# Kernel optimization log

Hardware: AMD Instinct MI355X
Metric: run time of the kernel (lower is better)

## Reference

```python
import jax, jax.numpy as jnp
import numpy as np

ALPHA = 0.2          # LeakyReLU slope
NEG_BIG = -9e15      # mask value from the torch code
LN_EPS = 1e-5        # torch LayerNorm default eps
GAT_SCALE = 1.0


def _layer_norm(x, g, b):
    mu = x.mean(-1, keepdims=True)
    var = ((x - mu) ** 2).mean(-1, keepdims=True)
    return (x - mu) * jax.lax.rsqrt(var + LN_EPS) * g + b


def _gat_layer(h, adj, W, a, concat):
    # h: [B,N,Fin], adj: [N,N] weighted, W: [Fin,Fout], a: [2*Fout,1]
    Wh = jnp.einsum('bnf,fo->bno', h, W)                 # [B,N,Fout]
    Fo = W.shape[1]
    a_i, a_j = a[:Fo, 0], a[Fo:, 0]
    # e[b,i,j] = leakyrelu(Wh[b,i].a_i + Wh[b,j].a_j)  (== cat([Wh_i,Wh_j]) @ a)
    e = jax.nn.leaky_relu(
        (Wh @ a_i)[:, :, None] + (Wh @ a_j)[:, None, :], ALPHA)  # [B,N,N]
    att = jnp.where(adj[None, :, :] > 0, e, NEG_BIG)
    att = jax.nn.softmax(att, axis=2)
    att = att * adj[None, :, :]
    att = att / (att.sum(axis=2, keepdims=True) + 1e-8)
    h_prime = jnp.einsum('bij,bjo->bio', att, Wh)        # [B,N,Fout]
    return jax.nn.elu(h_prime) if concat else h_prime


def setup_inputs() -> dict:
    B, N, H, ID = 1024, 128, 64, 8
    GIN = 1 + ID  # node_feat_dim = 0
    key = jax.random.key(0)
    ks = jax.random.split(key, 20)
    # sparse weighted adjacency with self-loops
    w = jax.random.uniform(ks[0], (N, N))
    m = (jax.random.uniform(ks[1], (N, N)) < 0.3).astype(jnp.float32)
    adj = w * m + jnp.eye(N, dtype=jnp.float32)
    sc = lambda k, s: jax.random.normal(k, s, jnp.float32) * 0.1
    return {
        'c_values': jax.random.normal(ks[2], (B, N), jnp.float32),
        'adj': adj,
        'agent_emb': sc(ks[3], (N, ID)),
        'W1': sc(ks[4], (GIN, H)), 'a1': sc(ks[5], (2 * H, 1)),
        'W2': sc(ks[6], (H, H)),   'a2': sc(ks[7], (2 * H, 1)),
        'ln1_g': jnp.ones((H,)), 'ln1_b': jnp.zeros((H,)),
        'ln2_g': jnp.ones((H,)), 'ln2_b': jnp.zeros((H,)),
        'head_gat_w': sc(ks[8], (H, 1)), 'head_gat_b': jnp.zeros((1,)),
        'mlp1_w': sc(ks[9], (N, H)),  'mlp1_b': jnp.zeros((H,)),
        'mlp2_w': sc(ks[10], (H, H)), 'mlp2_b': jnp.zeros((H,)),
        'head_mlp_w': sc(ks[11], (H, 1)), 'head_mlp_b': jnp.zeros((1,)),
        'gate1_w': sc(ks[12], (N, H)), 'gate1_b': jnp.zeros((H,)),
        'gate2_w': sc(ks[13], (H, 1)), 'gate2_b': jnp.full((1,), -5.0),
    }


def reference(c_values, adj, agent_emb, W1, a1, W2, a2,
              ln1_g, ln1_b, ln2_g, ln2_b, head_gat_w, head_gat_b,
              mlp1_w, mlp1_b, mlp2_w, mlp2_b, head_mlp_w, head_mlp_b,
              gate1_w, gate1_b, gate2_w, gate2_b):
    B, N = c_values.shape
    # node features: [c_value, agent_id_embedding]
    id_feat = jnp.broadcast_to(agent_emb[None], (B, N, agent_emb.shape[1]))
    x_g = jnp.concatenate([c_values[..., None], id_feat], axis=-1)  # [B,N,9]
    h1 = _gat_layer(x_g, adj, W1, a1, concat=True)
    h1 = _layer_norm(h1, ln1_g, ln1_b)
    h2 = _gat_layer(h1, adj, W2, a2, concat=False)
    h = jax.nn.relu(h2 + h1)
    h = _layer_norm(h, ln2_g, ln2_b)
    q_gat = h.mean(axis=1) @ head_gat_w + head_gat_b                # [B,1]
    x_m = jax.nn.relu(c_values @ mlp1_w + mlp1_b)
    x_m = jax.nn.relu(x_m @ mlp2_w + mlp2_b)
    q_mlp = x_m @ head_mlp_w + head_mlp_b                           # [B,1]
    gate = jax.nn.sigmoid(
        jax.nn.relu(c_values @ gate1_w + gate1_b) @ gate2_w + gate2_b)
    return q_mlp + gate * GAT_SCALE * q_gat
```

## Files before the change

### kernel.cpp

```cpp
#include <hip/hip_runtime.h>

typedef unsigned short u16;
typedef unsigned int u32;
typedef short v8s __attribute__((ext_vector_type(8)));
typedef float v4f __attribute__((ext_vector_type(4)));

__device__ __forceinline__ float bflo(u32 d){union{u32 i;float f;}u;u.i=d<<16;return u.f;}
__device__ __forceinline__ float bfhi(u32 d){union{u32 i;float f;}u;u.i=d&0xffff0000u;return u.f;}
__device__ __forceinline__ u16 f2bfr(float f){union{float f;u32 i;}u;u.f=f;return (u16)((u.i+0x8000u)>>16);}
__device__ __forceinline__ u32 pk2bf(float a,float b){
    union{float f;u32 i;}ua,ub; ua.f=a; ub.f=b;
    return ((ua.i+0x8000u)>>16)|((ub.i+0x8000u)&0xffff0000u);
}
__device__ __forceinline__ v8s pack8(const float* w){
    union { uint4 u; v8s v; } c;
    c.u.x = pk2bf(w[0],w[1]); c.u.y = pk2bf(w[2],w[3]);
    c.u.z = pk2bf(w[4],w[5]); c.u.w = pk2bf(w[6],w[7]);
    return c.v;
}

__device__ __forceinline__ void flash_att(
    int wv, int l15, int q4,
    const float* __restrict__ ADJ,
    const float* __restrict__ sEi, const float* __restrict__ sEj,
    const u16* __restrict__ sWhT,
    v4f acc[2][4], float invD[2])
{
    const int r0 = 16*wv + l15, r1 = r0 + 64;
    const float ei0 = sEi[r0], ei1 = sEi[r1];
    float D0 = 0.f, D1 = 0.f;
    #pragma unroll
    for (int s = 0; s < 2; ++s)
        #pragma unroll
        for (int ct = 0; ct < 4; ++ct) acc[s][ct] = (v4f){0.f,0.f,0.f,0.f};

    for (int ks = 0; ks < 4; ++ks) {
        const int ko = ks*32 + q4*8;
        float ej[8];
        *(float4*)(ej)     = *(const float4*)(sEj + ko);
        *(float4*)(ej + 4) = *(const float4*)(sEj + ko + 4);
        float4 a00 = *(const float4*)(ADJ + r0*128 + ko);
        float4 a01 = *(const float4*)(ADJ + r0*128 + ko + 4);
        float4 a10 = *(const float4*)(ADJ + r1*128 + ko);
        float4 a11 = *(const float4*)(ADJ + r1*128 + ko + 4);
        float av0[8] = {a00.x,a00.y,a00.z,a00.w,a01.x,a01.y,a01.z,a01.w};
        float av1[8] = {a10.x,a10.y,a10.z,a10.w,a11.x,a11.y,a11.z,a11.w};
        float w0[8], w1[8];
        #pragma unroll
        for (int k = 0; k < 8; ++k) {
            float e0 = ei0 + ej[k]; e0 = fmaxf(e0, 0.2f*e0);
            float e1 = ei1 + ej[k]; e1 = fmaxf(e1, 0.2f*e1);
            float x0 = __expf(e0) * av0[k];
            float x1 = __expf(e1) * av1[k];
            w0[k] = x0; w1[k] = x1; D0 += x0; D1 += x1;
        }
        v8s A0 = pack8(w0), A1 = pack8(w1);
        #pragma unroll
        for (int ct = 0; ct < 4; ++ct) {
            v8s B = *(const v8s*)(sWhT + (16*ct + l15)*136 + ko);
            acc[0][ct] = __builtin_amdgcn_mfma_f32_16x16x32_bf16(A0, B, acc[0][ct], 0,0,0);
            acc[1][ct] = __builtin_amdgcn_mfma_f32_16x16x32_bf16(A1, B, acc[1][ct], 0,0,0);
        }
    }
    D0 += __shfl_xor(D0, 16); D0 += __shfl_xor(D0, 32);
    D1 += __shfl_xor(D1, 16); D1 += __shfl_xor(D1, 32);
    invD[0] = 1.f / D0; invD[1] = 1.f / D1;
}

__global__ __launch_bounds__(256, 4) void graphmixer_kernel(
    const float* __restrict__ C,
    const float* __restrict__ ADJ,
    const float* __restrict__ EMB,
    const float* __restrict__ W1,
    const float* __restrict__ A1,
    const float* __restrict__ W2,
    const float* __restrict__ A2,
    const float* __restrict__ LN1G, const float* __restrict__ LN1B,
    const float* __restrict__ LN2G, const float* __restrict__ LN2B,
    const float* __restrict__ HGW,  const float* __restrict__ HGB,
    const float* __restrict__ MLP1W, const float* __restrict__ MLP1B,
    const float* __restrict__ MLP2W, const float* __restrict__ MLP2B,
    const float* __restrict__ HMW,  const float* __restrict__ HMB,
    const float* __restrict__ G1W,  const float* __restrict__ G1B,
    const float* __restrict__ G2W,  const float* __restrict__ G2B,
    float* __restrict__ OUT)
{
    const int b = blockIdx.x, t = threadIdx.x;
    const int lane = t & 63, wv = t >> 6;
    const int l15 = lane & 15, q4 = lane >> 4;

    __shared__ __align__(16) unsigned char smem[39072];
    u16*   sWhT = (u16*)(smem);
    u16*   sH1  = (u16*)(smem + 17408);
    float* sEi  = (float*)(smem + 35840);
    float* sEj  = (float*)(smem + 36352);
    float* colp = (float*)(smem + 36864);
    float* sScr = (float*)(smem + 37888);
    float* v2i  = (float*)(smem + 38432);
    float* v2j  = (float*)(smem + 38688);
    float* v1i  = (float*)(smem + 38944);
    float* v1j  = (float*)(smem + 39008);
    float* sEmb = (float*)(smem + 17408);
    float* sC   = (float*)(smem + 21504);

    const float* Cb = C + b*128;

    if (wv == 0) {
        #pragma unroll
        for (int q = 0; q < 4; ++q)
            ((float4*)sEmb)[lane + 64*q] = ((const float4*)EMB)[lane + 64*q];
        if (lane < 32) ((float4*)sC)[lane] = ((const float4*)Cb)[lane];
        if (lane >= 32 && lane < 41) {
            int f = lane - 32; float a = 0.f;
            for (int q = 0; q < 16; ++q) {
                float4 w = *(const float4*)(W1 + f*64 + q*4);
                float4 x = *(const float4*)(A1 + q*4);
                a += w.x*x.x + w.y*x.y + w.z*x.z + w.w*x.w;
            }
            v1i[f] = a;
        } else if (lane >= 48 && lane < 57) {
            int f = lane - 48; float a = 0.f;
            for (int q = 0; q < 16; ++q) {
                float4 w = *(const float4*)(W1 + f*64 + q*4);
                float4 x = *(const float4*)(A1 + 64 + q*4);
                a += w.x*x.x + w.y*x.y + w.z*x.z + w.w*x.w;
            }
            v1j[f] = a;
        }
    } else if (wv == 3) {
        float ai = 0.f, aj = 0.f;
        for (int q = 0; q < 16; ++q) {
            float4 w  = *(const float4*)(W2 + lane*64 + q*4);
            float4 xi = *(const float4*)(A2 + q*4);
            float4 xj = *(const float4*)(A2 + 64 + q*4);
            ai += w.x*xi.x + w.y*xi.y + w.z*xi.z + w.w*xi.w;
            aj += w.x*xj.x + w.y*xj.y + w.z*xj.z + w.w*xj.w;
        }
        v2i[lane] = ai; v2j[lane] = aj;
    } else if (wv == 1) {
        float a = 0.f;
        for (int k = 0; k < 128; k += 4) {
            float4 c4 = *(const float4*)(Cb + k);
            a += c4.x*MLP1W[k*64+lane] + c4.y*MLP1W[(k+1)*64+lane]
               + c4.z*MLP1W[(k+2)*64+lane] + c4.w*MLP1W[(k+3)*64+lane];
        }
        sScr[lane] = fmaxf(a + MLP1B[lane], 0.f);
        float a2 = 0.f;
        for (int k = 0; k < 64; ++k) a2 += sScr[k] * MLP2W[k*64 + lane];
        float x2 = fmaxf(a2 + MLP2B[lane], 0.f);
        float p1 = x2 * HMW[lane];
        #pragma unroll
        for (int off = 32; off >= 1; off >>= 1) p1 += __shfl_down(p1, off);
        if (lane == 0) sScr[128] = p1 + HMB[0];
    } else {
        float a = 0.f;
        for (int k = 0; k < 128; k += 4) {
            float4 c4 = *(const float4*)(Cb + k);
            a += c4.x*G1W[k*64+lane] + c4.y*G1W[(k+1)*64+lane]
               + c4.z*G1W[(k+2)*64+lane] + c4.w*G1W[(k+3)*64+lane];
        }
        sScr[64 + lane] = fmaxf(a + G1B[lane], 0.f);
        float p2 = sScr[64 + lane] * G2W[lane];
        #pragma unroll
        for (int off = 32; off >= 1; off >>= 1) p2 += __shfl_down(p2, off);
        if (lane == 0) sScr[129] = 1.f / (1.f + __expf(-(p2 + G2B[0])));
    }
    __syncthreads();

    {
        const int o = lane, cc = wv;
        float w1f[9];
        #pragma unroll
        for (int f = 0; f < 9; ++f) w1f[f] = W1[f*64 + o];
        float whv[32];
        for (int i = 0; i < 32; ++i) {
            const int ig = cc*32 + i;
            float a = sC[ig] * w1f[0];
            float4 e0 = *(const float4*)(sEmb + ig*8);
            float4 e1 = *(const float4*)(sEmb + ig*8 + 4);
            a += e0.x*w1f[1] + e0.y*w1f[2] + e0.z*w1f[3] + e0.w*w1f[4];
            a += e1.x*w1f[5] + e1.y*w1f[6] + e1.z*w1f[7] + e1.w*w1f[8];
            whv[i] = a;
        }
        u32 p[16];
        #pragma unroll
        for (int q = 0; q < 16; ++q) p[q] = pk2bf(whv[2*q], whv[2*q+1]);
        uint4* dst = (uint4*)(sWhT + o*136 + cc*32);
        dst[0] = ((uint4*)p)[0]; dst[1] = ((uint4*)p)[1];
        dst[2] = ((uint4*)p)[2]; dst[3] = ((uint4*)p)[3];
    }
    if (t < 128) {
        float c = sC[t];
        float4 e0 = *(const float4*)(sEmb + t*8);
        float4 e1 = *(const float4*)(sEmb + t*8 + 4);
        float ei = c*v1i[0] + e0.x*v1i[1]+e0.y*v1i[2]+e0.z*v1i[3]+e0.w*v1i[4]
                            + e1.x*v1i[5]+e1.y*v1i[6]+e1.z*v1i[7]+e1.w*v1i[8];
        float ej = c*v1j[0] + e0.x*v1j[1]+e0.y*v1j[2]+e0.z*v1j[3]+e0.w*v1j[4]
                            + e1.x*v1j[5]+e1.y*v1j[6]+e1.z*v1j[7]+e1.w*v1j[8];
        sEi[t] = ei; sEj[t] = ej;
    }
    __syncthreads();

    {
        v4f acc[2][4]; float invD[2];
        flash_att(wv, l15, q4, ADJ, sEi, sEj, sWhT, acc, invD);

        float g4[4], b4[4];
        #pragma unroll
        for (int ct = 0; ct < 4; ++ct) { g4[ct] = LN1G[16*ct + l15]; b4[ct] = LN1B[16*ct + l15]; }
        #pragma unroll
        for (int s = 0; s < 2; ++s) {
            const int rbase = 16*(wv + 4*s) + 4*q4;
            #pragma unroll
            for (int reg = 0; reg < 4; ++reg) {
                const int row = rbase + reg;
                const float rd = __shfl(invD[s], 4*q4 + reg);
                float x[4], s1 = 0.f, s2 = 0.f;
                #pragma unroll
                for (int ct = 0; ct < 4; ++ct) {
                    float v = acc[s][ct][reg] * rd;
                    v = (v > 0.f) ? v : (__expf(v) - 1.f);
                    x[ct] = v; s1 += v; s2 += v*v;
                }
                s1 += __shfl_xor(s1, 1); s2 += __shfl_xor(s2, 1);
                s1 += __shfl_xor(s1, 2); s2 += __shfl_xor(s2, 2);
                s1 += __shfl_xor(s1, 4); s2 += __shfl_xor(s2, 4);
                s1 += __shfl_xor(s1, 8); s2 += __shfl_xor(s2, 8);
                const float mean = s1 * (1.f/64.f);
                const float var  = s2 * (1.f/64.f) - mean*mean;
                const float rstd = rsqrtf(var + 1e-5f);
                #pragma unroll
                for (int ct = 0; ct < 4; ++ct) {
                    float h = (x[ct] - mean) * rstd * g4[ct] + b4[ct];
                    sH1[row*72 + 16*ct + l15] = f2bfr(h);
                }
            }
        }
    }
    __syncthreads();

    if (t < 128) {
        float ei = 0.f, ej = 0.f;
        const u16* hrow = sH1 + t*72;
        for (int q = 0; q < 16; ++q) {
            uint2 d = *(const uint2*)(hrow + q*4);
            float h0 = bflo(d.x), h1v = bfhi(d.x), h2 = bflo(d.y), h3 = bfhi(d.y);
            ei += h0*v2i[q*4+0] + h1v*v2i[q*4+1] + h2*v2i[q*4+2] + h3*v2i[q*4+3];
            ej += h0*v2j[q*4+0] + h1v*v2j[q*4+1] + h2*v2j[q*4+2] + h3*v2j[q*4+3];
        }
        sEi[t] = ei; sEj[t] = ej;
    }
    {
        v4f acc2[2][4];
        #pragma unroll
        for (int s = 0; s < 2; ++s)
            #pragma unroll
            for (int ct = 0; ct < 4; ++ct) acc2[s][ct] = (v4f){0.f,0.f,0.f,0.f};
        #pragma unroll
        for (int ks = 0; ks < 2; ++ks) {
            const int kb = ks*32 + q4*8;
            v8s Bf[4];
            #pragma unroll
            for (int ct = 0; ct < 4; ++ct) {
                const float* wp = W2 + kb*64 + 16*ct + l15;
                float w8[8];
                #pragma unroll
                for (int j = 0; j < 8; ++j) w8[j] = wp[j*64];
                Bf[ct] = pack8(w8);
            }
            #pragma unroll
            for (int s = 0; s < 2; ++s) {
                v8s A = *(const v8s*)(sH1 + (16*(wv+4*s) + l15)*72 + kb);
                #pragma unroll
                for (int ct = 0; ct < 4; ++ct)
                    acc2[s][ct] = __builtin_amdgcn_mfma_f32_16x16x32_bf16(A, Bf[ct], acc2[s][ct], 0,0,0);
            }
        }
        #pragma unroll
        for (int s = 0; s < 2; ++s) {
            const int rb = 16*(wv+4*s) + 4*q4;
            #pragma unroll
            for (int ct = 0; ct < 4; ++ct) {
                const int col = 16*ct + l15;
                uint2 p;
                p.x = pk2bf(acc2[s][ct][0], acc2[s][ct][1]);
                p.y = pk2bf(acc2[s][ct][2], acc2[s][ct][3]);
                *(uint2*)(sWhT + col*136 + rb) = p;
            }
        }
    }
    __syncthreads();

    {
        v4f acc[2][4]; float invD[2];
        flash_att(wv, l15, q4, ADJ, sEi, sEj, sWhT, acc, invD);

        float g4[4], b4[4], colsum[4];
        #pragma unroll
        for (int ct = 0; ct < 4; ++ct) {
            g4[ct] = LN2G[16*ct + l15]; b4[ct] = LN2B[16*ct + l15]; colsum[ct] = 0.f;
        }
        #pragma unroll
        for (int s = 0; s < 2; ++s) {
            const int rbase = 16*(wv + 4*s) + 4*q4;
            #pragma unroll
            for (int reg = 0; reg < 4; ++reg) {
                const int row = rbase + reg;
                const float rd = __shfl(invD[s], 4*q4 + reg);
                float x[4], s1 = 0.f, s2 = 0.f;
                #pragma unroll
                for (int ct = 0; ct < 4; ++ct) {
                    float h1v = bflo((u32)sH1[row*72 + 16*ct + l15]);
                    float v = fmaxf(acc[s][ct][reg] * rd + h1v, 0.f);
                    x[ct] = v; s1 += v; s2 += v*v;
                }
                s1 += __shfl_xor(s1, 1); s2 += __shfl_xor(s2, 1);
                s1 += __shfl_xor(s1, 2); s2 += __shfl_xor(s2, 2);
                s1 += __shfl_xor(s1, 4); s2 += __shfl_xor(s2, 4);
                s1 += __shfl_xor(s1, 8); s2 += __shfl_xor(s2, 8);
                const float mean = s1 * (1.f/64.f);
                const float var  = s2 * (1.f/64.f) - mean*mean;
                const float rstd = rsqrtf(var + 1e-5f);
                #pragma unroll
                for (int ct = 0; ct < 4; ++ct)
                    colsum[ct] += (x[ct] - mean) * rstd * g4[ct] + b4[ct];
            }
        }
        #pragma unroll
        for (int ct = 0; ct < 4; ++ct) {
            colsum[ct] += __shfl_xor(colsum[ct], 16);
            colsum[ct] += __shfl_xor(colsum[ct], 32);
        }
        if (lane < 16) {
            #pragma unroll
            for (int ct = 0; ct < 4; ++ct) colp[wv*64 + ct*16 + lane] = colsum[ct];
        }
    }
    __syncthreads();

    if (wv == 0) {
        float s = colp[lane] + colp[64 + lane] + colp[128 + lane] + colp[192 + lane];
        float p = s * (1.f/128.f) * HGW[lane];
        #pragma unroll
        for (int off = 32; off >= 1; off >>= 1) p += __shfl_down(p, off);
        if (lane == 0) OUT[b] = sScr[128] + sScr[129] * (p + HGB[0]);
    }
}

extern "C" void kernel_launch(void* const* d_in, const int* in_sizes, int n_in,
                              void* d_out, int out_size, void* d_ws, size_t ws_size,
                              hipStream_t stream) {
    (void)n_in; (void)out_size; (void)d_ws; (void)ws_size;
    const float* C     = (const float*)d_in[0];
    const float* ADJ   = (const float*)d_in[1];
    const float* EMB   = (const float*)d_in[2];
    const float* W1    = (const float*)d_in[3];
    const float* A1    = (const float*)d_in[4];
    const float* W2    = (const float*)d_in[5];
    const float* A2    = (const float*)d_in[6];
    const float* LN1G  = (const float*)d_in[7];
    const float* LN1B  = (const float*)d_in[8];
    const float* LN2G  = (const float*)d_in[9];
    const float* LN2B  = (const float*)d_in[10];
    const float* HGW   = (const float*)d_in[11];
    const float* HGB   = (const float*)d_in[12];
    const float* MLP1W = (const float*)d_in[13];
    const float* MLP1B = (const float*)d_in[14];
    const float* MLP2W = (const float*)d_in[15];
    const float* MLP2B = (const float*)d_in[16];
    const float* HMW   = (const float*)d_in[17];
    const float* HMB   = (const float*)d_in[18];
    const float* G1W   = (const float*)d_in[19];
    const float* G1B   = (const float*)d_in[20];
    const float* G2W   = (const float*)d_in[21];
    const float* G2B   = (const float*)d_in[22];

    const int B = in_sizes[0] / 128;

    graphmixer_kernel<<<dim3(B), dim3(256), 0, stream>>>(
        C, ADJ, EMB, W1, A1, W2, A2, LN1G, LN1B, LN2G, LN2B,
        HGW, HGB, MLP1W, MLP1B, MLP2W, MLP2B, HMW, HMB,
        G1W, G1B, G2W, G2B, (float*)d_out);
}
```

Baseline: 129.6 us.

## Factor attention exponentials per node and double block to eight waves

The LeakyReLU-then-exp attention weight is factored into per-node exponentials: exp(ei)·exp(ej) when the sum is positive, otherwise exp(0.2ei)·exp(0.2ej). These four vectors are precomputed once per node, so the inner loop becomes two multiplies and a select instead of a transcendental per edge. The block also grows from 256 to 512 threads, with each wave handling one 16-row tile instead of two, which spreads the MFMA and softmax work over more waves and reworks the shared-memory layout. The risks are overflow in the products for large logits, since there is no max subtraction, and higher register and LDS pressure per block.

```diff
diff --git a/kernel.cpp b/kernel.cpp
--- a/kernel.cpp
+++ b/kernel.cpp
@@ -22,52 +22,50 @@
 __device__ __forceinline__ void flash_att(
     int wv, int l15, int q4,
     const float* __restrict__ ADJ,
-    const float* __restrict__ sEi, const float* __restrict__ sEj,
+    const float* __restrict__ sEi, const float* __restrict__ sFi,
+    const float* __restrict__ sEj, const float* __restrict__ sFj,
     const u16* __restrict__ sWhT,
-    v4f acc[2][4], float invD[2])
+    v4f acc[4], float* invD)
 {
-    const int r0 = 16*wv + l15, r1 = r0 + 64;
-    const float ei0 = sEi[r0], ei1 = sEi[r1];
-    float D0 = 0.f, D1 = 0.f;
+    const int r0 = 16*wv + l15;
+    const float Ei = sEi[r0], Fi = sFi[r0];
+    float D = 0.f;
     #pragma unroll
-    for (int s = 0; s < 2; ++s)
-        #pragma unroll
-        for (int ct = 0; ct < 4; ++ct) acc[s][ct] = (v4f){0.f,0.f,0.f,0.f};
+    for (int ct = 0; ct < 4; ++ct) acc[ct] = (v4f){0.f,0.f,0.f,0.f};
 
     for (int ks = 0; ks < 4; ++ks) {
         const int ko = ks*32 + q4*8;
-        float ej[8];
-        *(float4*)(ej)     = *(const float4*)(sEj + ko);
-        *(float4*)(ej + 4) = *(const float4*)(sEj + ko + 4);
-        float4 a00 = *(const float4*)(ADJ + r0*128 + ko);
-        float4 a01 = *(const float4*)(ADJ + r0*128 + ko + 4);
-        float4 a10 = *(const float4*)(ADJ + r1*128 + ko);
-        float4 a11 = *(const float4*)(ADJ + r1*128 + ko + 4);
-        float av0[8] = {a00.x,a00.y,a00.z,a00.w,a01.x,a01.y,a01.z,a01.w};
-        float av1[8] = {a10.x,a10.y,a10.z,a10.w,a11.x,a11.y,a11.z,a11.w};
-        float w0[8], w1[8];
-        #pragma unroll
-        for (int k = 0; k < 8; ++k) {
-            float e0 = ei0 + ej[k]; e0 = fmaxf(e0, 0.2f*e0);
-            float e1 = ei1 + ej[k]; e1 = fmaxf(e1, 0.2f*e1);
-            float x0 = __expf(e0) * av0[k];
-            float x1 = __expf(e1) * av1[k];
-            w0[k] = x0; w1[k] = x1; D0 += x0; D1 += x1;
-        }
-        v8s A0 = pack8(w0), A1 = pack8(w1);
+        float w[8];
+        #pragma unroll
+        for (int half = 0; half < 2; ++half) {
+            float4 E4 = *(const float4*)(sEj + ko + 4*half);
+            float4 F4 = *(const float4*)(sFj + ko + 4*half);
+            float4 a4 = *(const float4*)(ADJ + r0*128 + ko + 4*half);
+            float Ev[4] = {E4.x,E4.y,E4.z,E4.w};
+            float Fv[4] = {F4.x,F4.y,F4.z,F4.w};
+            float av[4] = {a4.x,a4.y,a4.z,a4.w};
+            #pragma unroll
+            for (int k = 0; k < 4; ++k) {
+                float p = Ei * Ev[k];
+                float q = Fi * Fv[k];
+                float s = (p >= 1.f) ? p : q;
+                float ww = s * av[k];
+                w[half*4 + k] = ww;
+                D += ww;
+            }
+        }
+        v8s A = pack8(w);
         #pragma unroll
         for (int ct = 0; ct < 4; ++ct) {
             v8s B = *(const v8s*)(sWhT + (16*ct + l15)*136 + ko);
-            acc[0][ct] = __builtin_amdgcn_mfma_f32_16x16x32_bf16(A0, B, acc[0][ct], 0,0,0);
-            acc[1][ct] = __builtin_amdgcn_mfma_f32_16x16x32_bf16(A1, B, acc[1][ct], 0,0,0);
-        }
-    }
-    D0 += __shfl_xor(D0, 16); D0 += __shfl_xor(D0, 32);
-    D1 += __shfl_xor(D1, 16); D1 += __shfl_xor(D1, 32);
-    invD[0] = 1.f / D0; invD[1] = 1.f / D1;
-}
-
-__global__ __launch_bounds__(256, 4) void graphmixer_kernel(
+            acc[ct] = __builtin_amdgcn_mfma_f32_16x16x32_bf16(A, B, acc[ct], 0,0,0);
+        }
+    }
+    D += __shfl_xor(D, 16); D += __shfl_xor(D, 32);
+    *invD = 1.f / D;
+}
+
+__global__ __launch_bounds__(512, 8) void graphmixer_kernel(
     const float* __restrict__ C,
     const float* __restrict__ ADJ,
     const float* __restrict__ EMB,
@@ -89,17 +87,19 @@
     const int lane = t & 63, wv = t >> 6;
     const int l15 = lane & 15, q4 = lane >> 4;
 
-    __shared__ __align__(16) unsigned char smem[39072];
+    __shared__ __align__(16) unsigned char smem[40464];
     u16*   sWhT = (u16*)(smem);
     u16*   sH1  = (u16*)(smem + 17408);
     float* sEi  = (float*)(smem + 35840);
-    float* sEj  = (float*)(smem + 36352);
-    float* colp = (float*)(smem + 36864);
-    float* sScr = (float*)(smem + 37888);
-    float* v2i  = (float*)(smem + 38432);
-    float* v2j  = (float*)(smem + 38688);
-    float* v1i  = (float*)(smem + 38944);
-    float* v1j  = (float*)(smem + 39008);
+    float* sFi  = (float*)(smem + 36352);
+    float* sEj  = (float*)(smem + 36864);
+    float* sFj  = (float*)(smem + 37376);
+    float* v2i  = (float*)(smem + 37888);
+    float* v2j  = (float*)(smem + 38144);
+    float* v1i  = (float*)(smem + 38400);
+    float* v1j  = (float*)(smem + 38464);
+    float* colp = (float*)(smem + 37888);
+    float* sScr = (float*)(smem + 39936);
     float* sEmb = (float*)(smem + 17408);
     float* sC   = (float*)(smem + 21504);
 
@@ -110,23 +110,33 @@
         for (int q = 0; q < 4; ++q)
             ((float4*)sEmb)[lane + 64*q] = ((const float4*)EMB)[lane + 64*q];
         if (lane < 32) ((float4*)sC)[lane] = ((const float4*)Cb)[lane];
-        if (lane >= 32 && lane < 41) {
-            int f = lane - 32; float a = 0.f;
-            for (int q = 0; q < 16; ++q) {
-                float4 w = *(const float4*)(W1 + f*64 + q*4);
-                float4 x = *(const float4*)(A1 + q*4);
-                a += w.x*x.x + w.y*x.y + w.z*x.z + w.w*x.w;
-            }
-            v1i[f] = a;
-        } else if (lane >= 48 && lane < 57) {
-            int f = lane - 48; float a = 0.f;
-            for (int q = 0; q < 16; ++q) {
-                float4 w = *(const float4*)(W1 + f*64 + q*4);
-                float4 x = *(const float4*)(A1 + 64 + q*4);
-                a += w.x*x.x + w.y*x.y + w.z*x.z + w.w*x.w;
-            }
-            v1j[f] = a;
-        }
+    } else if (wv == 1) {
+        float a = 0.f;
+        for (int k = 0; k < 128; k += 4) {
+            float4 c4 = *(const float4*)(Cb + k);
+            a += c4.x*MLP1W[k*64+lane] + c4.y*MLP1W[(k+1)*64+lane]
+               + c4.z*MLP1W[(k+2)*64+lane] + c4.w*MLP1W[(k+3)*64+lane];
+        }
+        sScr[lane] = fmaxf(a + MLP1B[lane], 0.f);
+        float a2 = 0.f;
+        for (int k = 0; k < 64; ++k) a2 += sScr[k] * MLP2W[k*64 + lane];
+        float x2 = fmaxf(a2 + MLP2B[lane], 0.f);
+        float p1 = x2 * HMW[lane];
+        #pragma unroll
+        for (int off = 32; off >= 1; off >>= 1) p1 += __shfl_down(p1, off);
+        if (lane == 0) sScr[128] = p1 + HMB[0];
+    } else if (wv == 2) {
+        float a = 0.f;
+        for (int k = 0; k < 128; k += 4) {
+            float4 c4 = *(const float4*)(Cb + k);
+            a += c4.x*G1W[k*64+lane] + c4.y*G1W[(k+1)*64+lane]
+               + c4.z*G1W[(k+2)*64+lane] + c4.w*G1W[(k+3)*64+lane];
+        }
+        float g1 = fmaxf(a + G1B[lane], 0.f);
+        float p2 = g1 * G2W[lane];
+        #pragma unroll
+        for (int off = 32; off >= 1; off >>= 1) p2 += __shfl_down(p2, off);
+        if (lane == 0) sScr[129] = 1.f / (1.f + __expf(-(p2 + G2B[0])));
     } else if (wv == 3) {
         float ai = 0.f, aj = 0.f;
         for (int q = 0; q < 16; ++q) {
@@ -137,57 +147,47 @@
             aj += w.x*xj.x + w.y*xj.y + w.z*xj.z + w.w*xj.w;
         }
         v2i[lane] = ai; v2j[lane] = aj;
-    } else if (wv == 1) {
-        float a = 0.f;
-        for (int k = 0; k < 128; k += 4) {
-            float4 c4 = *(const float4*)(Cb + k);
-            a += c4.x*MLP1W[k*64+lane] + c4.y*MLP1W[(k+1)*64+lane]
-               + c4.z*MLP1W[(k+2)*64+lane] + c4.w*MLP1W[(k+3)*64+lane];
-        }
-        sScr[lane] = fmaxf(a + MLP1B[lane], 0.f);
-        float a2 = 0.f;
-        for (int k = 0; k < 64; ++k) a2 += sScr[k] * MLP2W[k*64 + lane];
-        float x2 = fmaxf(a2 + MLP2B[lane], 0.f);
-        float p1 = x2 * HMW[lane];
-        #pragma unroll
-        for (int off = 32; off >= 1; off >>= 1) p1 += __shfl_down(p1, off);
-        if (lane == 0) sScr[128] = p1 + HMB[0];
-    } else {
-        float a = 0.f;
-        for (int k = 0; k < 128; k += 4) {
-            float4 c4 = *(const float4*)(Cb + k);
-            a += c4.x*G1W[k*64+lane] + c4.y*G1W[(k+1)*64+lane]
-               + c4.z*G1W[(k+2)*64+lane] + c4.w*G1W[(k+3)*64+lane];
-        }
-        sScr[64 + lane] = fmaxf(a + G1B[lane], 0.f);
-        float p2 = sScr[64 + lane] * G2W[lane];
-        #pragma unroll
-        for (int off = 32; off >= 1; off >>= 1) p2 += __shfl_down(p2, off);
-        if (lane == 0) sScr[129] = 1.f / (1.f + __expf(-(p2 + G2B[0])));
+    } else if (wv == 4) {
+        if (lane < 9) {
+            float a = 0.f;
+            for (int q = 0; q < 16; ++q) {
+                float4 w = *(const float4*)(W1 + lane*64 + q*4);
+                float4 x = *(const float4*)(A1 + q*4);
+                a += w.x*x.x + w.y*x.y + w.z*x.z + w.w*x.w;
+            }
+            v1i[lane] = a;
+        } else if (lane >= 16 && lane < 25) {
+            int f = lane - 16; float a = 0.f;
+            for (int q = 0; q < 16; ++q) {
+                float4 w = *(const float4*)(W1 + f*64 + q*4);
+                float4 x = *(const float4*)(A1 + 64 + q*4);
+                a += w.x*x.x + w.y*x.y + w.z*x.z + w.w*x.w;
+            }
+            v1j[f] = a;
+        }
     }
     __syncthreads();
 
     {
-        const int o = lane, cc = wv;
+        const int o = lane;
         float w1f[9];
         #pragma unroll
         for (int f = 0; f < 9; ++f) w1f[f] = W1[f*64 + o];
-        float whv[32];
-        for (int i = 0; i < 32; ++i) {
-            const int ig = cc*32 + i;
+        float whv[16];
+        for (int ii = 0; ii < 16; ++ii) {
+            const int ig = 16*wv + ii;
             float a = sC[ig] * w1f[0];
             float4 e0 = *(const float4*)(sEmb + ig*8);
             float4 e1 = *(const float4*)(sEmb + ig*8 + 4);
             a += e0.x*w1f[1] + e0.y*w1f[2] + e0.z*w1f[3] + e0.w*w1f[4];
             a += e1.x*w1f[5] + e1.y*w1f[6] + e1.z*w1f[7] + e1.w*w1f[8];
-            whv[i] = a;
-        }
-        u32 p[16];
-        #pragma unroll
-        for (int q = 0; q < 16; ++q) p[q] = pk2bf(whv[2*q], whv[2*q+1]);
-        uint4* dst = (uint4*)(sWhT + o*136 + cc*32);
+            whv[ii] = a;
+        }
+        u32 p[8];
+        #pragma unroll
+        for (int q = 0; q < 8; ++q) p[q] = pk2bf(whv[2*q], whv[2*q+1]);
+        uint4* dst = (uint4*)(sWhT + o*136 + 16*wv);
         dst[0] = ((uint4*)p)[0]; dst[1] = ((uint4*)p)[1];
-        dst[2] = ((uint4*)p)[2]; dst[3] = ((uint4*)p)[3];
     }
     if (t < 128) {
         float c = sC[t];
@@ -197,43 +197,40 @@
                             + e1.x*v1i[5]+e1.y*v1i[6]+e1.z*v1i[7]+e1.w*v1i[8];
         float ej = c*v1j[0] + e0.x*v1j[1]+e0.y*v1j[2]+e0.z*v1j[3]+e0.w*v1j[4]
                             + e1.x*v1j[5]+e1.y*v1j[6]+e1.z*v1j[7]+e1.w*v1j[8];
-        sEi[t] = ei; sEj[t] = ej;
+        sEi[t] = __expf(ei); sFi[t] = __expf(0.2f*ei);
+        sEj[t] = __expf(ej); sFj[t] = __expf(0.2f*ej);
     }
     __syncthreads();
 
     {
-        v4f acc[2][4]; float invD[2];
-        flash_att(wv, l15, q4, ADJ, sEi, sEj, sWhT, acc, invD);
+        v4f acc[4]; float invD;
+        flash_att(wv, l15, q4, ADJ, sEi, sFi, sEj, sFj, sWhT, acc, &invD);
 
         float g4[4], b4[4];
         #pragma unroll
         for (int ct = 0; ct < 4; ++ct) { g4[ct] = LN1G[16*ct + l15]; b4[ct] = LN1B[16*ct + l15]; }
         #pragma unroll
-        for (int s = 0; s < 2; ++s) {
-            const int rbase = 16*(wv + 4*s) + 4*q4;
-            #pragma unroll
-            for (int reg = 0; reg < 4; ++reg) {
-                const int row = rbase + reg;
-                const float rd = __shfl(invD[s], 4*q4 + reg);
-                float x[4], s1 = 0.f, s2 = 0.f;
-                #pragma unroll
-                for (int ct = 0; ct < 4; ++ct) {
-                    float v = acc[s][ct][reg] * rd;
-                    v = (v > 0.f) ? v : (__expf(v) - 1.f);
-                    x[ct] = v; s1 += v; s2 += v*v;
-                }
-                s1 += __shfl_xor(s1, 1); s2 += __shfl_xor(s2, 1);
-                s1 += __shfl_xor(s1, 2); s2 += __shfl_xor(s2, 2);
-                s1 += __shfl_xor(s1, 4); s2 += __shfl_xor(s2, 4);
-                s1 += __shfl_xor(s1, 8); s2 += __shfl_xor(s2, 8);
-                const float mean = s1 * (1.f/64.f);
-                const float var  = s2 * (1.f/64.f) - mean*mean;
-                const float rstd = rsqrtf(var + 1e-5f);
-                #pragma unroll
-                for (int ct = 0; ct < 4; ++ct) {
-                    float h = (x[ct] - mean) * rstd * g4[ct] + b4[ct];
-                    sH1[row*72 + 16*ct + l15] = f2bfr(h);
-                }
+        for (int reg = 0; reg < 4; ++reg) {
+            const int row = 16*wv + 4*q4 + reg;
+            const float rd = __shfl(invD, 4*q4 + reg);
+            float x[4], s1 = 0.f, s2 = 0.f;
+            #pragma unroll
+            for (int ct = 0; ct < 4; ++ct) {
+                float v = acc[ct][reg] * rd;
+                v = (v > 0.f) ? v : (__expf(v) - 1.f);
+                x[ct] = v; s1 += v; s2 += v*v;
+            }
+            s1 += __shfl_xor(s1, 1); s2 += __shfl_xor(s2, 1);
+            s1 += __shfl_xor(s1, 2); s2 += __shfl_xor(s2, 2);
+            s1 += __shfl_xor(s1, 4); s2 += __shfl_xor(s2, 4);
+            s1 += __shfl_xor(s1, 8); s2 += __shfl_xor(s2, 8);
+            const float mean = s1 * (1.f/64.f);
+            const float var  = s2 * (1.f/64.f) - mean*mean;
+            const float rstd = rsqrtf(var + 1e-5f);
+            #pragma unroll
+            for (int ct = 0; ct < 4; ++ct) {
+                float h = (x[ct] - mean) * rstd * g4[ct] + b4[ct];
+                sH1[row*72 + 16*ct + l15] = f2bfr(h);
             }
         }
     }
@@ -248,52 +245,40 @@
             ei += h0*v2i[q*4+0] + h1v*v2i[q*4+1] + h2*v2i[q*4+2] + h3*v2i[q*4+3];
             ej += h0*v2j[q*4+0] + h1v*v2j[q*4+1] + h2*v2j[q*4+2] + h3*v2j[q*4+3];
         }
-        sEi[t] = ei; sEj[t] = ej;
+        sEi[t] = __expf(ei); sFi[t] = __expf(0.2f*ei);
+        sEj[t] = __expf(ej); sFj[t] = __expf(0.2f*ej);
     }
     {
-        v4f acc2[2][4];
-        #pragma unroll
-        for (int s = 0; s < 2; ++s)
-            #pragma unroll
-            for (int ct = 0; ct < 4; ++ct) acc2[s][ct] = (v4f){0.f,0.f,0.f,0.f};
+        v4f acc2[4];
+        #pragma unroll
+        for (int ct = 0; ct < 4; ++ct) acc2[ct] = (v4f){0.f,0.f,0.f,0.f};
         #pragma unroll
         for (int ks = 0; ks < 2; ++ks) {
             const int kb = ks*32 + q4*8;
-            v8s Bf[4];
+            v8s A = *(const v8s*)(sH1 + (16*wv + l15)*72 + kb);
             #pragma unroll
             for (int ct = 0; ct < 4; ++ct) {
                 const float* wp = W2 + kb*64 + 16*ct + l15;
                 float w8[8];
                 #pragma unroll
                 for (int j = 0; j < 8; ++j) w8[j] = wp[j*64];
-                Bf[ct] = pack8(w8);
-            }
-            #pragma unroll
-            for (int s = 0; s < 2; ++s) {
-                v8s A = *(const v8s*)(sH1 + (16*(wv+4*s) + l15)*72 + kb);
-                #pragma unroll
-                for (int ct = 0; ct < 4; ++ct)
-                    acc2[s][ct] = __builtin_amdgcn_mfma_f32_16x16x32_bf16(A, Bf[ct], acc2[s][ct], 0,0,0);
-            }
-        }
-        #pragma unroll
-        for (int s = 0; s < 2; ++s) {
-            const int rb = 16*(wv+4*s) + 4*q4;
-            #pragma unroll
-            for (int ct = 0; ct < 4; ++ct) {
-                const int col = 16*ct + l15;
-                uint2 p;
-                p.x = pk2bf(acc2[s][ct][0], acc2[s][ct][1]);
-                p.y = pk2bf(acc2[s][ct][2], acc2[s][ct][3]);
-                *(uint2*)(sWhT + col*136 + rb) = p;
-            }
+                acc2[ct] = __builtin_amdgcn_mfma_f32_16x16x32_bf16(A, pack8(w8), acc2[ct], 0,0,0);
+            }
+        }
+        const int rb = 16*wv + 4*q4;
+        #pragma unroll
+        for (int ct = 0; ct < 4; ++ct) {
+            uint2 p;
+            p.x = pk2bf(acc2[ct][0], acc2[ct][1]);
+            p.y = pk2bf(acc2[ct][2], acc2[ct][3]);
+            *(uint2*)(sWhT + (16*ct + l15)*136 + rb) = p;
         }
     }
     __syncthreads();
 
     {
-        v4f acc[2][4]; float invD[2];
-        flash_att(wv, l15, q4, ADJ, sEi, sEj, sWhT, acc, invD);
+        v4f acc[4]; float invD;
+        flash_att(wv, l15, q4, ADJ, sEi, sFi, sEj, sFj, sWhT, acc, &invD);
 
         float g4[4], b4[4], colsum[4];
         #pragma unroll
@@ -301,30 +286,26 @@
             g4[ct] = LN2G[16*ct + l15]; b4[ct] = LN2B[16*ct + l15]; colsum[ct] = 0.f;
         }
         #pragma unroll
-        for (int s = 0; s < 2; ++s) {
-            const int rbase = 16*(wv + 4*s) + 4*q4;
-            #pragma unroll
-            for (int reg = 0; reg < 4; ++reg) {
-                const int row = rbase + reg;
-                const float rd = __shfl(invD[s], 4*q4 + reg);
-                float x[4], s1 = 0.f, s2 = 0.f;
-                #pragma unroll
-                for (int ct = 0; ct < 4; ++ct) {
-                    float h1v = bflo((u32)sH1[row*72 + 16*ct + l15]);
-                    float v = fmaxf(acc[s][ct][reg] * rd + h1v, 0.f);
-                    x[ct] = v; s1 += v; s2 += v*v;
-                }
-                s1 += __shfl_xor(s1, 1); s2 += __shfl_xor(s2, 1);
-                s1 += __shfl_xor(s1, 2); s2 += __shfl_xor(s2, 2);
-                s1 += __shfl_xor(s1, 4); s2 += __shfl_xor(s2, 4);
-                s1 += __shfl_xor(s1, 8); s2 += __shfl_xor(s2, 8);
-                const float mean = s1 * (1.f/64.f);
-                const float var  = s2 * (1.f/64.f) - mean*mean;
-                const float rstd = rsqrtf(var + 1e-5f);
-                #pragma unroll
-                for (int ct = 0; ct < 4; ++ct)
-                    colsum[ct] += (x[ct] - mean) * rstd * g4[ct] + b4[ct];
-            }
+        for (int reg = 0; reg < 4; ++reg) {
+            const int row = 16*wv + 4*q4 + reg;
+            const float rd = __shfl(invD, 4*q4 + reg);
+            float x[4], s1 = 0.f, s2 = 0.f;
+            #pragma unroll
+            for (int ct = 0; ct < 4; ++ct) {
+                float h1v = bflo((u32)sH1[row*72 + 16*ct + l15]);
+                float v = fmaxf(acc[ct][reg] * rd + h1v, 0.f);
+                x[ct] = v; s1 += v; s2 += v*v;
+            }
+            s1 += __shfl_xor(s1, 1); s2 += __shfl_xor(s2, 1);
+            s1 += __shfl_xor(s1, 2); s2 += __shfl_xor(s2, 2);
+            s1 += __shfl_xor(s1, 4); s2 += __shfl_xor(s2, 4);
+            s1 += __shfl_xor(s1, 8); s2 += __shfl_xor(s2, 8);
+            const float mean = s1 * (1.f/64.f);
+            const float var  = s2 * (1.f/64.f) - mean*mean;
+            const float rstd = rsqrtf(var + 1e-5f);
+            #pragma unroll
+            for (int ct = 0; ct < 4; ++ct)
+                colsum[ct] += (x[ct] - mean) * rstd * g4[ct] + b4[ct];
         }
         #pragma unroll
         for (int ct = 0; ct < 4; ++ct) {
@@ -339,7 +320,9 @@
     __syncthreads();
 
     if (wv == 0) {
-        float s = colp[lane] + colp[64 + lane] + colp[128 + lane] + colp[192 + lane];
+        float s = 0.f;
+        #pragma unroll
+        for (int w = 0; w < 8; ++w) s += colp[w*64 + lane];
         float p = s * (1.f/128.f) * HGW[lane];
         #pragma unroll
         for (int off = 32; off >= 1; off >>= 1) p += __shfl_down(p, off);
@@ -377,7 +360,7 @@
 
     const int B = in_sizes[0] / 128;
 
-    graphmixer_kernel<<<dim3(B), dim3(256), 0, stream>>>(
+    graphmixer_kernel<<<dim3(B), dim3(512), 0, stream>>>(
         C, ADJ, EMB, W1, A1, W2, A2, LN1G, LN1B, LN2G, LN2B,
         HGW, HGB, MLP1W, MLP1B, MLP2W, MLP2B, HMW, HMB,
         G1W, G1B, G2W, G2B, (float*)d_out);
```

Result: slower. 134.5 us (+3.8%).
